# Kernel optimization log

Measured on AMD Instinct MI355X. Metric: run time of the kernel, lower is better.

## Reference

```python
import jax, jax.numpy as jnp
import numpy as np

NUM_NODES = 9746   # in_c
NUM_USER = 6040
HID_C = 500
OUT_C = 75
NUM_REL = 5
NUM_EDGES = 200000
NUM_BASIS = 2


def setup_inputs() -> dict:
    key = jax.random.key(0)
    ks = jax.random.split(key, 8)
    x = jnp.arange(NUM_NODES, dtype=jnp.int64)
    edge_index = jax.random.randint(ks[0], (2, NUM_EDGES), 0, NUM_NODES, dtype=jnp.int64)
    edge_type = jax.random.randint(ks[1], (NUM_EDGES,), 0, NUM_REL, dtype=jnp.int64)
    edge_norm = jax.random.uniform(ks[2], (NUM_EDGES,), dtype=jnp.float32)
    # learned params (random_init(0.001, .) ~ small uniform init)
    ord_basis = jax.random.normal(ks[3], (NUM_REL, NUM_NODES * HID_C), dtype=jnp.float32) * 0.001
    fc_w = jax.random.normal(ks[4], (OUT_C, HID_C), dtype=jnp.float32) * 0.001
    basis_matrix = jax.random.normal(ks[5], (NUM_BASIS, OUT_C * OUT_C), dtype=jnp.float32) * 0.001
    coefs = jax.random.normal(ks[6], (NUM_REL, NUM_BASIS), dtype=jnp.float32) * 0.001
    return {"x": x, "edge_index": edge_index, "edge_type": edge_type,
            "edge_norm": edge_norm, "ord_basis": ord_basis, "fc_w": fc_w,
            "basis_matrix": basis_matrix, "coefs": coefs}


def reference(x, edge_index, edge_type, edge_norm, ord_basis, fc_w, basis_matrix, coefs):
    # --- RGCLayer: cumulative ordinal basis weights -> gather -> relu -> scale -> scatter-add
    # weight[r] = sum_{r' <= r} ord_basis[r']  (the cat(weight, weight[-1]+basis) loop)
    weight = jnp.cumsum(ord_basis, axis=0).reshape(NUM_REL * NUM_NODES, HID_C)
    # drop_prob = 0 -> node_dropout mask is all ones (identity)
    src, dst = edge_index[0], edge_index[1]
    idx = edge_type * NUM_NODES + x[src]                  # [E] embedding-style index
    msg = jax.nn.relu(weight[idx]) * edge_norm[:, None]    # [E, HID_C]
    feats = jax.ops.segment_sum(msg, dst, num_segments=NUM_NODES)  # [N, HID_C]
    # --- DenseLayer (shared linear, no bias, dropout is identity)
    u = feats[:NUM_USER] @ fc_w.T                          # [U, OUT_C]
    i = feats[NUM_USER:] @ fc_w.T                          # [I, OUT_C]
    # --- BiDecoder: per-relation bilinear score, log_softmax over relations
    Q = jnp.einsum('rb,bf->rf', coefs, basis_matrix).reshape(NUM_REL, OUT_C, OUT_C)
    scores = jnp.einsum('uf,rfg,ig->uir', u, Q, i)         # [U, I, R]
    out = jax.nn.log_softmax(scores.reshape(-1, NUM_REL), axis=1)
    return out
```

## Files before the change

### kernel.cpp

```cpp
#include <hip/hip_runtime.h>

#define NNODES 9746
#define NUSER  6040
#define NITEM  3706
#define HIDC   500
#define OUTC   75
#define NREL   5
#define NEDGES 200000
#define NW     (NNODES * HIDC)

typedef unsigned short u16;
typedef unsigned int   u32;
typedef __attribute__((ext_vector_type(8))) short short8;
typedef __attribute__((ext_vector_type(4))) float f32x4;
typedef __attribute__((ext_vector_type(2))) float f32x2;

__device__ __forceinline__ u16 f2b(float f) {
    union { float f; u32 i; } v; v.f = f;
    u32 r = (v.i + 0x7FFFu + ((v.i >> 16) & 1u)) >> 16;
    return (u16)r;
}
__device__ __forceinline__ u32 pack2(float lo, float hi) {
    return (u32)f2b(lo) | ((u32)f2b(hi) << 16);
}

__global__ __launch_bounds__(256) void k_prep(
        const float* __restrict__ fcw, const float* __restrict__ coefs,
        const float* __restrict__ bm, const int* __restrict__ ei,
        u32* __restrict__ fcwB, float* __restrict__ Q,
        int* __restrict__ cursors, int* __restrict__ bucket) {
    int b = blockIdx.x;
    if (b < 80) {
        int o = b;
        int cp = threadIdx.x;
        float lo = 0.f, hi = 0.f;
        if (o < OUTC) {
            int c0 = 2 * cp;
            if (c0 < HIDC)     lo = fcw[o * HIDC + c0];
            if (c0 + 1 < HIDC) hi = fcw[o * HIDC + c0 + 1];
        }
        fcwB[o * 256 + cp] = pack2(lo, hi);
    } else if (b < 190) {
        int j = (b - 80) * 256 + threadIdx.x;
        if (j < NREL * OUTC * OUTC) {
            int r = j / (OUTC * OUTC);
            int f = j - r * (OUTC * OUTC);
            Q[j] = coefs[2 * r] * bm[f] + coefs[2 * r + 1] * bm[OUTC * OUTC + f];
        }
    } else {
        int e = (b - 190) * 256 + threadIdx.x;
        if (e < NEDGES) {
            int d = ei[NEDGES + e];
            int pos = atomicAdd(&cursors[d], 1);
            if (pos < 64) bucket[d * 64 + pos] = e;
        }
    }
}

#define YBOFF 2560
__global__ __launch_bounds__(320) void k_y(const float* __restrict__ ord,
                                           const u32* __restrict__ fcwB,
                                           float* __restrict__ Y) {
    __shared__ u32 smem[5120];
    const int tid = threadIdx.x;
    const int s0 = blockIdx.x * 16;
    const int wv = tid / 64;
    const int lane = tid & 63;
    const int m = lane & 15;
    const int q = lane >> 4;

    const int as = tid >> 4;
    const int acp = tid & 15;

    f32x4 acc[5];
    #pragma unroll
    for (int r = 0; r < 5; ++r) acc[r] = (f32x4)0.f;

    for (int kc = 0; kc < 16; ++kc) {
        __syncthreads();
        if (tid < 256) {
            int c0 = kc * 32 + 2 * acp;
            float cx = 0.f, cy = 0.f;
            int aoff = as * 32 + 4 * ((acp >> 2) ^ (as & 7)) + (acp & 3);
            bool okc = (c0 < HIDC) && (s0 + as < NNODES);
            const float* op = ord + (size_t)(s0 + as) * HIDC + c0;
            #pragma unroll
            for (int r = 0; r < 5; ++r) {
                if (okc) {
                    float2 v = *(const float2*)(op + (size_t)r * NW);
                    cx += v.x; cy += v.y;
                }
                smem[r * 512 + aoff] = pack2(fmaxf(cx, 0.f), fmaxf(cy, 0.f));
            }
        }
        for (int j = tid; j < 1280; j += 320) {
            int o = j >> 4, cp = j & 15;
            smem[YBOFF + o * 32 + 4 * ((cp >> 2) ^ (o & 7)) + (cp & 3)]
                = fcwB[o * 256 + kc * 16 + cp];
        }
        __syncthreads();

        int co = 4 * (q ^ (m & 7));
        short8 bvv = *(const short8*)&smem[YBOFF + (wv * 16 + m) * 32 + co];
        #pragma unroll
        for (int r = 0; r < 5; ++r) {
            short8 av = *(const short8*)&smem[(r * 16 + m) * 32 + co];
            acc[r] = __builtin_amdgcn_mfma_f32_16x16x32_bf16(av, bvv, acc[r], 0, 0, 0);
        }
    }

    #pragma unroll
    for (int j = 0; j < 4; ++j) {
        int s = s0 + q * 4 + j;
        if (s < NNODES) {
            #pragma unroll
            for (int r = 0; r < 5; ++r)
                Y[((size_t)r * NNODES + s) * 80 + wv * 16 + m] = acc[r][j];
        }
    }
}

__global__ __launch_bounds__(512) void k_ga(
        const int* __restrict__ ei, const int* __restrict__ etype,
        const float* __restrict__ enorm, const float* __restrict__ Y,
        const int* __restrict__ cursors, const int* __restrict__ bucket,
        const float* __restrict__ Q,
        u32* __restrict__ Abf, u32* __restrict__ zbf) {
    __shared__ int   s_src[8][64];
    __shared__ int   s_r[8][64];
    __shared__ float s_n[8][64];
    __shared__ float zs[8][80];
    __shared__ float asf[8][5][80];
    const int tid = threadIdx.x;
    const int w = tid >> 6;
    const int lane = tid & 63;
    const int b = blockIdx.x;
    const int dst = b * 8 + w;

    int deg = (dst < NNODES) ? cursors[dst] : 0;
    if (deg > 64) deg = 64;
    if (lane < deg) {
        int e = bucket[dst * 64 + lane];
        s_src[w][lane] = ei[e];
        s_r[w][lane]   = etype[e];
        s_n[w][lane]   = enorm[e];
    }
    __syncthreads();

    if (lane < 20) {
        float4 acc = make_float4(0.f, 0.f, 0.f, 0.f);
        if (deg > 0) {
            float4 cur = *((const float4*)(Y + ((size_t)s_r[w][0] * NNODES + s_src[w][0]) * 80) + lane);
            for (int p = 1; p < deg; ++p) {
                float4 nxt = *((const float4*)(Y + ((size_t)s_r[w][p] * NNODES + s_src[w][p]) * 80) + lane);
                float nrm = s_n[w][p - 1];
                acc.x += nrm * cur.x; acc.y += nrm * cur.y;
                acc.z += nrm * cur.z; acc.w += nrm * cur.w;
                cur = nxt;
            }
            float nrm = s_n[w][deg - 1];
            acc.x += nrm * cur.x; acc.y += nrm * cur.y;
            acc.z += nrm * cur.z; acc.w += nrm * cur.w;
        }
        *(float4*)&zs[w][lane * 4] = acc;
    }
    __syncthreads();

    if (b < 755) {
        if (tid < NREL * OUTC) {
            int r = tid / OUTC, g = tid - r * OUTC;
            float acc[8] = {};
            for (int f = 0; f < OUTC; ++f) {
                float qv = Q[(r * OUTC + f) * OUTC + g];
                #pragma unroll
                for (int u = 0; u < 8; ++u) acc[u] += zs[u][f] * qv;
            }
            #pragma unroll
            for (int u = 0; u < 8; ++u) asf[u][r][g] = acc[u];
        }
        __syncthreads();
        const int u0 = b * 8;
        for (int j = tid; j < 8 * 5 * 48; j += 512) {
            int u = j / 240; int rem = j - u * 240;
            int r = rem / 48; int wd = rem - r * 48;
            int g0 = 2 * wd;
            float lo = (g0 < OUTC) ? asf[u][r][g0] : 0.f;
            float hi = (g0 + 1 < OUTC) ? asf[u][r][g0 + 1] : 0.f;
            Abf[((size_t)(u0 + u) * 5 + r) * 48 + wd] = pack2(lo, hi);
        }
    } else {
        const int i0 = b * 8 - NUSER;
        for (int j = tid; j < 8 * 48; j += 512) {
            int u = j / 48; int wd = j - u * 48;
            int i = i0 + u;
            if (i < 3712) {
                int g0 = 2 * wd;
                float lo = 0.f, hi = 0.f;
                if (i < NITEM) {
                    if (g0 < OUTC)     lo = zs[u][g0];
                    if (g0 + 1 < OUTC) hi = zs[u][g0 + 1];
                }
                zbf[(size_t)i * 48 + wd] = pack2(lo, hi);
            }
        }
    }
}

#define BOFF 5120
#define OROW 648
__global__ __launch_bounds__(256) void k_scores(const u32* __restrict__ Abf,
                                                const u32* __restrict__ zbf,
                                                float* __restrict__ out) {
    __shared__ u32 smem[13312];
    float* smf = (float*)smem;
    const int tid = threadIdx.x;
    const int utile = blockIdx.x * 16;
    const int itile = blockIdx.y * 128;

    const uint4* Ag = (const uint4*)Abf;
    for (int j = tid; j < 960; j += 256) {
        int u = j / 60; int rem = j - u * 60;
        int r = rem / 12; int w4 = rem - r * 12;
        uint4 v = make_uint4(0u, 0u, 0u, 0u);
        if (utile + u < NUSER) v = Ag[((size_t)(utile + u) * 5 + r) * 12 + w4];
        *(uint4*)&smem[(r * 16 + u) * 64 + 4 * (w4 ^ (u & 7))] = v;
    }
    const uint4* Bg = (const uint4*)zbf;
    for (int j = tid; j < 1536; j += 256) {
        int i = j / 12; int w4 = j - i * 12;
        *(uint4*)&smem[BOFF + i * 64 + 4 * (w4 ^ (i & 7))] = Bg[(size_t)(itile + i) * 12 + w4];
    }
    __syncthreads();

    const int lane = tid & 63;
    const int wv = tid >> 6;
    const int m = lane & 15;
    const int q = lane >> 4;
    const int sw = m & 7;

    f32x4 acc[2][5];
    #pragma unroll
    for (int fi = 0; fi < 2; ++fi)
        #pragma unroll
        for (int r = 0; r < 5; ++r) acc[fi][r] = (f32x4)0.f;

    #pragma unroll
    for (int kc = 0; kc < 3; ++kc) {
        int c = kc * 4 + q;
        int co = 4 * (c ^ sw);
        short8 av[5], bv[2];
        #pragma unroll
        for (int r = 0; r < 5; ++r)
            av[r] = *(const short8*)&smem[(r * 16 + m) * 64 + co];
        #pragma unroll
        for (int fi = 0; fi < 2; ++fi)
            bv[fi] = *(const short8*)&smem[BOFF + (wv * 32 + fi * 16 + m) * 64 + co];
        #pragma unroll
        for (int fi = 0; fi < 2; ++fi)
            #pragma unroll
            for (int r = 0; r < 5; ++r)
                acc[fi][r] = __builtin_amdgcn_mfma_f32_16x16x32_bf16(
                    av[r], bv[fi], acc[fi][r], 0, 0, 0);
    }
    __syncthreads();

    #pragma unroll
    for (int fi = 0; fi < 2; ++fi) {
        int i_loc = wv * 32 + fi * 16 + m;
        #pragma unroll
        for (int j = 0; j < 4; ++j) {
            int u_loc = q * 4 + j;
            float v0 = acc[fi][0][j], v1 = acc[fi][1][j], v2 = acc[fi][2][j],
                  v3 = acc[fi][3][j], v4 = acc[fi][4][j];
            float mx = fmaxf(fmaxf(fmaxf(v0, v1), fmaxf(v2, v3)), v4);
            float ss = __expf(v0 - mx) + __expf(v1 - mx) + __expf(v2 - mx)
                     + __expf(v3 - mx) + __expf(v4 - mx);
            float lse = mx + __logf(ss);
            float* d = smf + u_loc * OROW + 2 * ((utile + u_loc) & 1) + i_loc * 5;
            d[0] = v0 - lse; d[1] = v1 - lse; d[2] = v2 - lse;
            d[3] = v3 - lse; d[4] = v4 - lse;
        }
    }
    __syncthreads();

    int uvalid = NUSER - utile; if (uvalid > 16) uvalid = 16;
    int ivalid = NITEM - itile; if (ivalid > 128) ivalid = 128;
    const int F = ivalid * 5;
    for (int j = tid; j < uvalid * 160; j += 256) {
        int u = j / 160; int k = j - u * 160;
        int sh = (utile + u) & 1;
        int Nq = (F - 2 * sh) >> 2;
        if (k < Nq) {
            size_t gbase = (size_t)(utile + u) * (NITEM * 5) + (size_t)itile * 5;
            f32x4 v = *(const f32x4*)&smf[u * OROW + 4 * sh + 4 * k];
            __builtin_nontemporal_store(v, (f32x4*)(out + gbase + 2 * sh + 4 * k));
        }
    }
    if (tid < uvalid) {
        int u = tid;
        int sh = (utile + u) & 1;
        size_t gbase = (size_t)(utile + u) * (NITEM * 5) + (size_t)itile * 5;
        if (sh) {
            f32x2 h = *(const f32x2*)&smf[u * OROW + 2];
            __builtin_nontemporal_store(h, (f32x2*)(out + gbase));
        }
        int Nq = (F - 2 * sh) >> 2;
        if (((F - 2 * sh) & 3) != 0) {
            int t0 = 2 * sh + 4 * Nq;
            f32x2 tl = *(const f32x2*)&smf[u * OROW + 2 * sh + t0];
            __builtin_nontemporal_store(tl, (f32x2*)(out + gbase + t0));
        }
    }
}

extern "C" void kernel_launch(void* const* d_in, const int* in_sizes, int n_in,
                              void* d_out, int out_size, void* d_ws, size_t ws_size,
                              hipStream_t stream) {
    const int*   ei    = (const int*)d_in[1];
    const int*   etype = (const int*)d_in[2];
    const float* enorm = (const float*)d_in[3];
    const float* ord   = (const float*)d_in[4];
    const float* fcw   = (const float*)d_in[5];
    const float* bm    = (const float*)d_in[6];
    const float* coefs = (const float*)d_in[7];
    float* out = (float*)d_out;

    int*   ws_i    = (int*)d_ws;
    int*   cursors = ws_i + 0;
    int*   bucket  = ws_i + 9748;
    u32*   fcwB    = (u32*)(ws_i + 633496);
    float* Q       = (float*)(ws_i + 653976);
    float* Y       = (float*)(ws_i + 682104);
    u32*   Abf     = (u32*)(ws_i + 4580504);
    u32*   zbf     = (u32*)(ws_i + 6030104);

    (void)hipMemsetAsync(cursors, 0, 9746 * sizeof(int), stream);

    k_prep<<<972, 256, 0, stream>>>(fcw, coefs, bm, ei, fcwB, Q, cursors, bucket);
    k_y<<<(NNODES + 15) / 16, 320, 0, stream>>>(ord, fcwB, Y);
    k_ga<<<1219, 512, 0, stream>>>(ei, etype, enorm, Y, cursors, bucket, Q, Abf, zbf);
    dim3 sg((NUSER + 15) / 16, (NITEM + 127) / 128);
    k_scores<<<sg, 256, 0, stream>>>(Abf, zbf, out);
}
```

Before: 675.2 us.

## Fuse prep into Y kernel and loop item tiles inside persistent score blocks

Merges the prep kernel (Q build and edge bucketing) into the Y-projection kernel as extra blocks, and converts fcw to bf16 on the fly instead of staging a packed copy, removing one launch and one intermediate buffer. The scores kernel now launches one block per 16-user tile and loops over all 29 item tiles, keeping the user A-fragment resident in LDS instead of reloading it per block. The trade-off is much less grid parallelism for the output-write-bound scores kernel (378 blocks instead of about 11k), and fcw is re-read and converted by every Y block.

```diff
diff --git a/kernel.cpp b/kernel.cpp
--- a/kernel.cpp
+++ b/kernel.cpp
@@ -24,51 +24,39 @@
     return (u32)f2b(lo) | ((u32)f2b(hi) << 16);
 }
 
-__global__ __launch_bounds__(256) void k_prep(
-        const float* __restrict__ fcw, const float* __restrict__ coefs,
-        const float* __restrict__ bm, const int* __restrict__ ei,
-        u32* __restrict__ fcwB, float* __restrict__ Q,
-        int* __restrict__ cursors, int* __restrict__ bucket) {
-    int b = blockIdx.x;
-    if (b < 80) {
-        int o = b;
-        int cp = threadIdx.x;
-        float lo = 0.f, hi = 0.f;
-        if (o < OUTC) {
-            int c0 = 2 * cp;
-            if (c0 < HIDC)     lo = fcw[o * HIDC + c0];
-            if (c0 + 1 < HIDC) hi = fcw[o * HIDC + c0 + 1];
-        }
-        fcwB[o * 256 + cp] = pack2(lo, hi);
-    } else if (b < 190) {
-        int j = (b - 80) * 256 + threadIdx.x;
-        if (j < NREL * OUTC * OUTC) {
-            int r = j / (OUTC * OUTC);
-            int f = j - r * (OUTC * OUTC);
-            Q[j] = coefs[2 * r] * bm[f] + coefs[2 * r + 1] * bm[OUTC * OUTC + f];
-        }
-    } else {
-        int e = (b - 190) * 256 + threadIdx.x;
-        if (e < NEDGES) {
+#define YBOFF 2560
+__global__ __launch_bounds__(320) void k_py(
+        const float* __restrict__ ord, const float* __restrict__ fcw,
+        const float* __restrict__ coefs, const float* __restrict__ bm,
+        const int* __restrict__ ei,
+        float* __restrict__ Q, int* __restrict__ cursors,
+        int* __restrict__ bucket, float* __restrict__ Y) {
+    __shared__ u32 smem[5120];
+    const int b = blockIdx.x;
+    const int tid = threadIdx.x;
+
+    if (b >= 610) {
+        if (b < 698) {
+            int j = (b - 610) * 320 + tid;
+            if (j < NREL * OUTC * OUTC) {
+                int r = j / (OUTC * OUTC);
+                int f = j - r * (OUTC * OUTC);
+                Q[j] = coefs[2 * r] * bm[f] + coefs[2 * r + 1] * bm[OUTC * OUTC + f];
+            }
+        } else {
+            int e = (b - 698) * 320 + tid;
             int d = ei[NEDGES + e];
             int pos = atomicAdd(&cursors[d], 1);
             if (pos < 64) bucket[d * 64 + pos] = e;
         }
-    }
-}
-
-#define YBOFF 2560
-__global__ __launch_bounds__(320) void k_y(const float* __restrict__ ord,
-                                           const u32* __restrict__ fcwB,
-                                           float* __restrict__ Y) {
-    __shared__ u32 smem[5120];
-    const int tid = threadIdx.x;
-    const int s0 = blockIdx.x * 16;
+        return;
+    }
+
+    const int s0 = b * 16;
     const int wv = tid / 64;
     const int lane = tid & 63;
     const int m = lane & 15;
     const int q = lane >> 4;
-
     const int as = tid >> 4;
     const int acp = tid & 15;
 
@@ -95,8 +83,10 @@
         }
         for (int j = tid; j < 1280; j += 320) {
             int o = j >> 4, cp = j & 15;
-            smem[YBOFF + o * 32 + 4 * ((cp >> 2) ^ (o & 7)) + (cp & 3)]
-                = fcwB[o * 256 + kc * 16 + cp];
+            int c0 = 2 * (kc * 16 + cp);
+            float2 v = make_float2(0.f, 0.f);
+            if (o < OUTC && c0 < HIDC) v = *(const float2*)(fcw + o * HIDC + c0);
+            smem[YBOFF + o * 32 + 4 * ((cp >> 2) ^ (o & 7)) + (cp & 3)] = pack2(v.x, v.y);
         }
         __syncthreads();
 
@@ -206,16 +196,16 @@
     }
 }
 
-#define BOFF 5120
+#define UOFF 5120
 #define OROW 648
 __global__ __launch_bounds__(256) void k_scores(const u32* __restrict__ Abf,
                                                 const u32* __restrict__ zbf,
                                                 float* __restrict__ out) {
-    __shared__ u32 smem[13312];
-    float* smf = (float*)smem;
+    __shared__ u32 smem[15488];
+    u32* Bs = smem + UOFF;
+    float* smf = (float*)(smem + UOFF);
     const int tid = threadIdx.x;
     const int utile = blockIdx.x * 16;
-    const int itile = blockIdx.y * 128;
 
     const uint4* Ag = (const uint4*)Abf;
     for (int j = tid; j < 960; j += 256) {
@@ -225,90 +215,94 @@
         if (utile + u < NUSER) v = Ag[((size_t)(utile + u) * 5 + r) * 12 + w4];
         *(uint4*)&smem[(r * 16 + u) * 64 + 4 * (w4 ^ (u & 7))] = v;
     }
-    const uint4* Bg = (const uint4*)zbf;
-    for (int j = tid; j < 1536; j += 256) {
-        int i = j / 12; int w4 = j - i * 12;
-        *(uint4*)&smem[BOFF + i * 64 + 4 * (w4 ^ (i & 7))] = Bg[(size_t)(itile + i) * 12 + w4];
-    }
-    __syncthreads();
 
     const int lane = tid & 63;
     const int wv = tid >> 6;
     const int m = lane & 15;
     const int q = lane >> 4;
     const int sw = m & 7;
-
-    f32x4 acc[2][5];
-    #pragma unroll
-    for (int fi = 0; fi < 2; ++fi)
-        #pragma unroll
-        for (int r = 0; r < 5; ++r) acc[fi][r] = (f32x4)0.f;
-
-    #pragma unroll
-    for (int kc = 0; kc < 3; ++kc) {
-        int c = kc * 4 + q;
-        int co = 4 * (c ^ sw);
-        short8 av[5], bv[2];
-        #pragma unroll
-        for (int r = 0; r < 5; ++r)
-            av[r] = *(const short8*)&smem[(r * 16 + m) * 64 + co];
+    int uvalid = NUSER - utile; if (uvalid > 16) uvalid = 16;
+
+    const uint4* Bg = (const uint4*)zbf;
+    for (int it = 0; it < 29; ++it) {
+        const int itile = it * 128;
+        __syncthreads();
+        for (int j = tid; j < 1536; j += 256) {
+            int i = j / 12; int w4 = j - i * 12;
+            *(uint4*)&Bs[i * 64 + 4 * (w4 ^ (i & 7))] = Bg[(size_t)(itile + i) * 12 + w4];
+        }
+        __syncthreads();
+
+        f32x4 acc[2][5];
         #pragma unroll
         for (int fi = 0; fi < 2; ++fi)
-            bv[fi] = *(const short8*)&smem[BOFF + (wv * 32 + fi * 16 + m) * 64 + co];
+            #pragma unroll
+            for (int r = 0; r < 5; ++r) acc[fi][r] = (f32x4)0.f;
+
         #pragma unroll
-        for (int fi = 0; fi < 2; ++fi)
+        for (int kc = 0; kc < 3; ++kc) {
+            int co = 4 * ((kc * 4 + q) ^ sw);
+            short8 av[5], bv[2];
             #pragma unroll
             for (int r = 0; r < 5; ++r)
-                acc[fi][r] = __builtin_amdgcn_mfma_f32_16x16x32_bf16(
-                    av[r], bv[fi], acc[fi][r], 0, 0, 0);
-    }
-    __syncthreads();
-
-    #pragma unroll
-    for (int fi = 0; fi < 2; ++fi) {
-        int i_loc = wv * 32 + fi * 16 + m;
+                av[r] = *(const short8*)&smem[(r * 16 + m) * 64 + co];
+            #pragma unroll
+            for (int fi = 0; fi < 2; ++fi)
+                bv[fi] = *(const short8*)&Bs[(wv * 32 + fi * 16 + m) * 64 + co];
+            #pragma unroll
+            for (int fi = 0; fi < 2; ++fi)
+                #pragma unroll
+                for (int r = 0; r < 5; ++r)
+                    acc[fi][r] = __builtin_amdgcn_mfma_f32_16x16x32_bf16(
+                        av[r], bv[fi], acc[fi][r], 0, 0, 0);
+        }
+        __syncthreads();
+
         #pragma unroll
-        for (int j = 0; j < 4; ++j) {
-            int u_loc = q * 4 + j;
-            float v0 = acc[fi][0][j], v1 = acc[fi][1][j], v2 = acc[fi][2][j],
-                  v3 = acc[fi][3][j], v4 = acc[fi][4][j];
-            float mx = fmaxf(fmaxf(fmaxf(v0, v1), fmaxf(v2, v3)), v4);
-            float ss = __expf(v0 - mx) + __expf(v1 - mx) + __expf(v2 - mx)
-                     + __expf(v3 - mx) + __expf(v4 - mx);
-            float lse = mx + __logf(ss);
-            float* d = smf + u_loc * OROW + 2 * ((utile + u_loc) & 1) + i_loc * 5;
-            d[0] = v0 - lse; d[1] = v1 - lse; d[2] = v2 - lse;
-            d[3] = v3 - lse; d[4] = v4 - lse;
-        }
-    }
-    __syncthreads();
-
-    int uvalid = NUSER - utile; if (uvalid > 16) uvalid = 16;
-    int ivalid = NITEM - itile; if (ivalid > 128) ivalid = 128;
-    const int F = ivalid * 5;
-    for (int j = tid; j < uvalid * 160; j += 256) {
-        int u = j / 160; int k = j - u * 160;
-        int sh = (utile + u) & 1;
-        int Nq = (F - 2 * sh) >> 2;
-        if (k < Nq) {
+        for (int fi = 0; fi < 2; ++fi) {
+            int i_loc = wv * 32 + fi * 16 + m;
+            #pragma unroll
+            for (int j = 0; j < 4; ++j) {
+                int u_loc = q * 4 + j;
+                float v0 = acc[fi][0][j], v1 = acc[fi][1][j], v2 = acc[fi][2][j],
+                      v3 = acc[fi][3][j], v4 = acc[fi][4][j];
+                float mx = fmaxf(fmaxf(fmaxf(v0, v1), fmaxf(v2, v3)), v4);
+                float ss = __expf(v0 - mx) + __expf(v1 - mx) + __expf(v2 - mx)
+                         + __expf(v3 - mx) + __expf(v4 - mx);
+                float lse = mx + __logf(ss);
+                float* d = smf + u_loc * OROW + 2 * ((utile + u_loc) & 1) + i_loc * 5;
+                d[0] = v0 - lse; d[1] = v1 - lse; d[2] = v2 - lse;
+                d[3] = v3 - lse; d[4] = v4 - lse;
+            }
+        }
+        __syncthreads();
+
+        const int ivalid = (it == 28) ? (NITEM - itile) : 128;
+        const int F = ivalid * 5;
+        for (int j = tid; j < uvalid * 160; j += 256) {
+            int u = j / 160; int k = j - u * 160;
+            int sh = (utile + u) & 1;
+            int Nq = (F - 2 * sh) >> 2;
+            if (k < Nq) {
+                size_t gbase = (size_t)(utile + u) * (NITEM * 5) + (size_t)itile * 5;
+                f32x4 v = *(const f32x4*)&smf[u * OROW + 4 * sh + 4 * k];
+                __builtin_nontemporal_store(v, (f32x4*)(out + gbase + 2 * sh + 4 * k));
+            }
+        }
+        if (tid < uvalid) {
+            int u = tid;
+            int sh = (utile + u) & 1;
             size_t gbase = (size_t)(utile + u) * (NITEM * 5) + (size_t)itile * 5;
-            f32x4 v = *(const f32x4*)&smf[u * OROW + 4 * sh + 4 * k];
-            __builtin_nontemporal_store(v, (f32x4*)(out + gbase + 2 * sh + 4 * k));
-        }
-    }
-    if (tid < uvalid) {
-        int u = tid;
-        int sh = (utile + u) & 1;
-        size_t gbase = (size_t)(utile + u) * (NITEM * 5) + (size_t)itile * 5;
-        if (sh) {
-            f32x2 h = *(const f32x2*)&smf[u * OROW + 2];
-            __builtin_nontemporal_store(h, (f32x2*)(out + gbase));
-        }
-        int Nq = (F - 2 * sh) >> 2;
-        if (((F - 2 * sh) & 3) != 0) {
-            int t0 = 2 * sh + 4 * Nq;
-            f32x2 tl = *(const f32x2*)&smf[u * OROW + 2 * sh + t0];
-            __builtin_nontemporal_store(tl, (f32x2*)(out + gbase + t0));
+            if (sh) {
+                f32x2 h = *(const f32x2*)&smf[u * OROW + 2];
+                __builtin_nontemporal_store(h, (f32x2*)(out + gbase));
+            }
+            int Nq = (F - 2 * sh) >> 2;
+            if (((F - 2 * sh) & 3) != 0) {
+                int t0 = 2 * sh + 4 * Nq;
+                f32x2 tl = *(const f32x2*)&smf[u * OROW + 2 * sh + t0];
+                __builtin_nontemporal_store(tl, (f32x2*)(out + gbase + t0));
+            }
         }
     }
 }
@@ -328,17 +322,14 @@
     int*   ws_i    = (int*)d_ws;
     int*   cursors = ws_i + 0;
     int*   bucket  = ws_i + 9748;
-    u32*   fcwB    = (u32*)(ws_i + 633496);
-    float* Q       = (float*)(ws_i + 653976);
-    float* Y       = (float*)(ws_i + 682104);
-    u32*   Abf     = (u32*)(ws_i + 4580504);
-    u32*   zbf     = (u32*)(ws_i + 6030104);
+    float* Q       = (float*)(ws_i + 633496);
+    float* Y       = (float*)(ws_i + 661624);
+    u32*   Abf     = (u32*)(ws_i + 4560024);
+    u32*   zbf     = (u32*)(ws_i + 6009624);
 
     (void)hipMemsetAsync(cursors, 0, 9746 * sizeof(int), stream);
 
-    k_prep<<<972, 256, 0, stream>>>(fcw, coefs, bm, ei, fcwB, Q, cursors, bucket);
-    k_y<<<(NNODES + 15) / 16, 320, 0, stream>>>(ord, fcwB, Y);
+    k_py<<<1323, 320, 0, stream>>>(ord, fcw, coefs, bm, ei, Q, cursors, bucket, Y);
     k_ga<<<1219, 512, 0, stream>>>(ei, etype, enorm, Y, cursors, bucket, Q, Abf, zbf);
-    dim3 sg((NUSER + 15) / 16, (NITEM + 127) / 128);
-    k_scores<<<sg, 256, 0, stream>>>(Abf, zbf, out);
-}
+    k_scores<<<378, 256, 0, stream>>>(Abf, zbf, out);
+}
```

Result: slower. 724.7 us (+7.3%).
